# Performance work log

Hardware: AMD Instinct MI355X
Metric: run time of the kernel (lower is better)

Reference implementation:

```python
import jax, jax.numpy as jnp
import numpy as np

N = 100_000
E = 1_600_000
F_IN, D1, D2, D_EMB = 64, 32, 64, 64
NUM_GRAPHS = 16
BN_EPS = 1e-5


def _glorot(key, shape):
    fan_in, fan_out = shape[0], shape[1]
    lim = (6.0 / (fan_in + fan_out)) ** 0.5
    return jax.random.uniform(key, shape, jnp.float32, -lim, lim)


def setup_inputs() -> dict:
    key = jax.random.key(0)
    ks = jax.random.split(key, 12)
    x = jax.random.normal(ks[0], (N, F_IN), jnp.float32)
    edge_index = jax.random.randint(ks[1], (2, E), 0, N, jnp.int64)
    batch = jnp.sort(jax.random.randint(ks[2], (N,), 0, NUM_GRAPHS, jnp.int64))
    return {
        "x": x,
        "edge_index": edge_index,
        "batch": batch,
        "num_graphs": NUM_GRAPHS,
        "num_nodes": N,
        "W1a": _glorot(ks[3], (F_IN, D1)), "b1a": jnp.zeros((D1,), jnp.float32),
        "W1b": _glorot(ks[4], (D1, D2)), "b1b": jnp.zeros((D2,), jnp.float32),
        "g1": jnp.ones((D2,), jnp.float32), "be1": jnp.zeros((D2,), jnp.float32),
        "W2a": _glorot(ks[5], (D2, D2)), "b2a": jnp.zeros((D2,), jnp.float32),
        "W2b": _glorot(ks[6], (D2, D_EMB)), "b2b": jnp.zeros((D_EMB,), jnp.float32),
        "g2": jnp.ones((D_EMB,), jnp.float32), "be2": jnp.zeros((D_EMB,), jnp.float32),
    }


def _batchnorm_train(h, gamma, beta):
    mean = jnp.mean(h, axis=0)
    var = jnp.mean(jnp.square(h - mean), axis=0)  # biased var, as torch BN uses for normalization
    return (h - mean) * jax.lax.rsqrt(var + BN_EPS) * gamma + beta


def _gin_aggregate(x, src, dst, valid, n_nodes):
    # sum_{j in N(i)} x_j over valid edges only (masked scatter-add)
    msg = x[src] * valid[:, None]  # [E, D]
    return jax.ops.segment_sum(msg, dst, num_segments=n_nodes)


def reference(x, edge_index, batch, num_graphs, num_nodes,
              W1a, b1a, W1b, b1b, g1, be1,
              W2a, b2a, W2b, b2b, g2, be2):
    n_edges = edge_index.shape[1]
    per = n_edges // num_graphs
    # edge_mask: per-edge threshold g * num_nodes / num_graphs applied to both rows
    thresh = jnp.repeat(jnp.arange(num_graphs), per).astype(jnp.float32) * (num_nodes / num_graphs)
    valid = jnp.all(edge_index.astype(jnp.float32) - thresh[None, :] >= 0.0, axis=0)
    valid = valid.astype(x.dtype)
    src, dst = edge_index[0], edge_index[1]

    # GINConv 1 (eps=0): nn1(x + aggr)
    h = x + _gin_aggregate(x, src, dst, valid, num_nodes)
    h = jax.nn.relu(h @ W1a + b1a) @ W1b + b1b
    h = jax.nn.relu(h)
    h = _batchnorm_train(h, g1, be1)

    # GINConv 2
    h = h + _gin_aggregate(h, src, dst, valid, num_nodes)
    h = jax.nn.relu(h @ W2a + b2a) @ W2b + b2b
    h = jax.nn.relu(h)
    h = _batchnorm_train(h, g2, be2)

    # global_mean_pool
    sums = jax.ops.segment_sum(h, batch, num_segments=num_graphs)
    counts = jax.ops.segment_sum(jnp.ones((h.shape[0],), h.dtype), batch, num_segments=num_graphs)
    return sums / jnp.maximum(counts, 1.0)[:, None]
```

## Files before the change

### kernel.cpp

```cpp
#include <hip/hip_runtime.h>
#include <hip/hip_fp16.h>

#define NG 16
#define D 64
#define SLOT 32
#define NPB 128
#define INH 72

union HF4 { float4 f4; __half2 h2[4]; };
union HF2 { float2 f2; __half2 h2[2]; };

typedef _Float16 half4_t __attribute__((ext_vector_type(4)));
typedef float float4_t __attribute__((ext_vector_type(4)));

__device__ __forceinline__ float2 f2fma(float2 a, float2 b, float2 c) {
  return make_float2(fmaf(a.x, b.x, c.x), fmaf(a.y, b.y, c.y));
}
__device__ __forceinline__ float2 f2add(float2 a, float2 b) {
  return make_float2(a.x + b.x, a.y + b.y);
}

__global__ void prep_kernel(const float* __restrict__ x,
                            float2* __restrict__ xh, int n4,
                            float4* __restrict__ xz, float4* __restrict__ hz,
                            const int* __restrict__ ei,
                            int* __restrict__ fill, int* __restrict__ col,
                            int E, int per, int tmul) {
  int t = blockIdx.x * 256 + threadIdx.x;
  if (blockIdx.x == 0 && threadIdx.x < 16) {
    float4 z = make_float4(0.f, 0.f, 0.f, 0.f);
    if (threadIdx.x < 8) xz[threadIdx.x] = z;
    else hz[threadIdx.x - 8] = z;
  }
  if (t < n4) {
    float4 v = ((const float4*)x)[t];
    HF2 u;
    u.h2[0] = __floats2half2_rn(v.x, v.y);
    u.h2[1] = __floats2half2_rn(v.z, v.w);
    xh[t] = u.f2;
  }
  if (t < E) {
    int src = ei[t];
    int dst = ei[E + t];
    int thr = (t / per) * tmul;
    if (src >= thr && dst >= thr) {
      int k = atomicAdd(&fill[dst], 1);
      if (k < SLOT) col[dst * SLOT + k] = src;
    }
  }
}

template <int MID, bool FOLD_BN, int EPI>
__global__ __launch_bounds__(512, 2) void fused_layer_kernel(
    const float4* __restrict__ feat4,
    const int* __restrict__ col, const int* __restrict__ deg,
    const float* __restrict__ bn_sum, const float* __restrict__ bn_sq,
    const float* __restrict__ bn_gamma, const float* __restrict__ bn_beta,
    float invN,
    const float* __restrict__ Wa, const float* __restrict__ ba,
    const float* __restrict__ Wb, const float* __restrict__ bb,
    float2* __restrict__ out2,
    const int* __restrict__ batch,
    float* __restrict__ st_sum,
    float* __restrict__ st_sq,
    float* __restrict__ cnt,
    int N) {
  constexpr int CT = MID / 16;

  __shared__ __align__(16) __half s_h[NPB * INH];
  __shared__ __align__(16) __half s_wa[MID * 64];
  __shared__ __align__(16) __half s_wb[64 * MID];
  __shared__ __align__(16) float s_ba[MID];
  __shared__ __align__(16) float s_bb[D];
  __shared__ float s_bna[FOLD_BN ? D : 1];
  __shared__ float s_bnb[FOLD_BN ? D : 1];
  __shared__ int s_cnt[2];

  int tid = threadIdx.x;
  int base = blockIdx.x * NPB;

  {
    constexpr int WA_SLOTS = MID * 16;
    constexpr int WB_SLOTS = MID * 16;
    for (int g = tid; g < WA_SLOTS + WB_SLOTS; g += 512) {
      half4_t v;
      if (g < WA_SLOTS) {
        int l = g & 63, kt = (g >> 6) & 3, ct = g >> 8;
        int k0 = kt * 16 + ((l >> 4) << 2);
        int c = ct * 16 + (l & 15);
#pragma unroll
        for (int i = 0; i < 4; i++) v[i] = (_Float16)Wa[(k0 + i) * MID + c];
        *(half4_t*)&s_wa[g * 4] = v;
      } else {
        int g2 = g - WA_SLOTS;
        int l = g2 & 63;
        int kt = (g2 >> 6) & (CT - 1);
        int ot = g2 >> (6 + (CT == 4 ? 2 : 1));
        int k0 = kt * 16 + ((l >> 4) << 2);
        int o = ot * 16 + (l & 15);
#pragma unroll
        for (int i = 0; i < 4; i++) v[i] = (_Float16)Wb[(k0 + i) * D + o];
        *(half4_t*)&s_wb[g2 * 4] = v;
      }
    }
  }
  if (tid < MID) s_ba[tid] = ba[tid];
  if (tid < D) s_bb[tid] = bb[tid];
  if (FOLD_BN && tid < D) {
    float mean = bn_sum[tid] * invN;
    float var = bn_sq[tid] * invN - mean * mean;
    float av = bn_gamma[tid] * rsqrtf(var + 1e-5f);
    s_bna[tid] = av;
    s_bnb[tid] = bn_beta[tid] - mean * av;
  }
  if (EPI == 2 && tid < 2) s_cnt[tid] = 0;
  __syncthreads();

  {
    int q8 = tid & 7;
#pragma unroll
    for (int s0 = 0; s0 < 2; s0++) {
      int slot = (tid >> 3) + 64 * s0;
      int node = base + slot;
      float2 acc[4];
      if (node < N) {
        int d = min(deg[node], SLOT);
        const int* cl = col + node * SLOT;
        {
          HF4 s; s.f4 = feat4[(size_t)node * 8 + q8];
#pragma unroll
          for (int i = 0; i < 4; i++) acc[i] = __half22float2(s.h2[i]);
        }
        int dpad = (d + 15) & ~15;
        for (int j = 0; j < dpad; j += 16) {
          int4 sa = *(const int4*)(cl + j);
          int4 sb = *(const int4*)(cl + j + 4);
          int4 sc = *(const int4*)(cl + j + 8);
          int4 sd = *(const int4*)(cl + j + 12);
          int idx[16];
          idx[0]  = (j + 0  < d) ? sa.x : N;  idx[1]  = (j + 1  < d) ? sa.y : N;
          idx[2]  = (j + 2  < d) ? sa.z : N;  idx[3]  = (j + 3  < d) ? sa.w : N;
          idx[4]  = (j + 4  < d) ? sb.x : N;  idx[5]  = (j + 5  < d) ? sb.y : N;
          idx[6]  = (j + 6  < d) ? sb.z : N;  idx[7]  = (j + 7  < d) ? sb.w : N;
          idx[8]  = (j + 8  < d) ? sc.x : N;  idx[9]  = (j + 9  < d) ? sc.y : N;
          idx[10] = (j + 10 < d) ? sc.z : N;  idx[11] = (j + 11 < d) ? sc.w : N;
          idx[12] = (j + 12 < d) ? sd.x : N;  idx[13] = (j + 13 < d) ? sd.y : N;
          idx[14] = (j + 14 < d) ? sd.z : N;  idx[15] = (j + 15 < d) ? sd.w : N;
          HF4 u[16];
#pragma unroll
          for (int i = 0; i < 16; i++) u[i].f4 = feat4[(size_t)idx[i] * 8 + q8];
#pragma unroll
          for (int i = 0; i < 16; i++) {
#pragma unroll
            for (int c = 0; c < 4; c++)
              acc[c] = f2add(acc[c], __half22float2(u[i].h2[c]));
          }
        }
        if (FOLD_BN) {
          float dp = (float)(d + 1);
          int c0 = q8 * 8;
#pragma unroll
          for (int c = 0; c < 4; c++) {
            float2 a2 = *(const float2*)&s_bna[c0 + 2 * c];
            float2 b2 = *(const float2*)&s_bnb[c0 + 2 * c];
            acc[c] = f2fma(a2, acc[c], make_float2(dp * b2.x, dp * b2.y));
          }
        }
      } else {
#pragma unroll
        for (int i = 0; i < 4; i++) acc[i] = make_float2(0.f, 0.f);
      }
      HF4 o;
#pragma unroll
      for (int c = 0; c < 4; c++)
        o.h2[c] = __floats2half2_rn(acc[c].x, acc[c].y);
      *(float4*)&s_h[slot * INH + q8 * 8] = o.f4;
    }
  }
  __syncthreads();

  int w = tid >> 6;
  int l = tid & 63;
  int lg = l >> 4;
  int ln = l & 15;
  int nodeB = base + w * 16 + ln;

  half4_t hb[4];
#pragma unroll
  for (int kt = 0; kt < 4; kt++)
    hb[kt] = *(const half4_t*)&s_h[(w * 16 + ln) * INH + kt * 16 + lg * 4];

  float4_t c1[CT];
#pragma unroll
  for (int ct = 0; ct < CT; ct++) {
    c1[ct] = *(const float4_t*)&s_ba[ct * 16 + lg * 4];
#pragma unroll
    for (int kt = 0; kt < 4; kt++) {
      half4_t a = *(const half4_t*)&s_wa[((ct * 4 + kt) * 64 + l) * 4];
      c1[ct] = __builtin_amdgcn_mfma_f32_16x16x16f16(a, hb[kt], c1[ct], 0, 0, 0);
    }
  }
  half4_t mb[CT];
#pragma unroll
  for (int ct = 0; ct < CT; ct++) {
#pragma unroll
    for (int r = 0; r < 4; r++) mb[ct][r] = (_Float16)fmaxf(c1[ct][r], 0.f);
  }
  float4_t o4[4];
#pragma unroll
  for (int ot = 0; ot < 4; ot++) {
    o4[ot] = *(const float4_t*)&s_bb[ot * 16 + lg * 4];
#pragma unroll
    for (int kt = 0; kt < CT; kt++) {
      half4_t a = *(const half4_t*)&s_wb[((ot * CT + kt) * 64 + l) * 4];
      o4[ot] = __builtin_amdgcn_mfma_f32_16x16x16f16(a, mb[kt], o4[ot], 0, 0, 0);
    }
#pragma unroll
    for (int r = 0; r < 4; r++) o4[ot][r] = fmaxf(o4[ot][r], 0.f);
  }

  float* red = (float*)s_h;

  if (EPI == 1) {
    bool val = nodeB < N;
    if (val) {
#pragma unroll
      for (int ot = 0; ot < 4; ot++) {
        HF2 u;
        u.h2[0] = __floats2half2_rn(o4[ot][0], o4[ot][1]);
        u.h2[1] = __floats2half2_rn(o4[ot][2], o4[ot][3]);
        out2[(size_t)nodeB * 16 + ot * 4 + lg] = u.f2;
      }
    }
    float vm = val ? 1.f : 0.f;
#pragma unroll
    for (int ot = 0; ot < 4; ot++) {
      float4_t s, q;
#pragma unroll
      for (int r = 0; r < 4; r++) {
        float x = vm * o4[ot][r];
        s[r] = x; q[r] = x * o4[ot][r];
      }
#pragma unroll
      for (int m = 1; m < 16; m <<= 1) {
#pragma unroll
        for (int r = 0; r < 4; r++) {
          s[r] += __shfl_xor(s[r], m);
          q[r] += __shfl_xor(q[r], m);
        }
      }
      if (ln == 0) {
        *(float4_t*)&red[w * 576 + ot * 16 + lg * 4] = s;
        *(float4_t*)&red[w * 576 + 64 + ot * 16 + lg * 4] = q;
      }
    }
    __syncthreads();
    if (tid < D) {
      float s = 0.f, q = 0.f;
#pragma unroll
      for (int ww = 0; ww < 8; ww++) {
        s += red[ww * 576 + tid];
        q += red[ww * 576 + 64 + tid];
      }
      atomicAdd(&st_sum[tid], s);
      atomicAdd(&st_sq[tid], q);
    }
  }

  if (EPI == 2) {
    bool val = nodeB < N;
    int bl = val ? batch[nodeB] : -1;
    int g_lo = batch[base];
    int g_hi = batch[min(base + NPB - 1, N - 1)];
    float vm = val ? 1.f : 0.f;
    float wlo = (bl == g_lo) ? 1.f : 0.f;
    unsigned long long mlo = __ballot(lg == 0 && bl == g_lo);
    unsigned long long mhi = __ballot(lg == 0 && val && bl != g_lo);
    if (l == 0) {
      atomicAdd(&s_cnt[0], (int)__popcll(mlo));
      atomicAdd(&s_cnt[1], (int)__popcll(mhi));
    }
#pragma unroll
    for (int ot = 0; ot < 4; ot++) {
      float4_t sl, st, sq;
#pragma unroll
      for (int r = 0; r < 4; r++) {
        float x = vm * o4[ot][r];
        sl[r] = wlo * x;
        st[r] = x;
        sq[r] = x * o4[ot][r];
      }
#pragma unroll
      for (int m = 1; m < 16; m <<= 1) {
#pragma unroll
        for (int r = 0; r < 4; r++) {
          sl[r] += __shfl_xor(sl[r], m);
          st[r] += __shfl_xor(st[r], m);
          sq[r] += __shfl_xor(sq[r], m);
        }
      }
      if (ln == 0) {
        *(float4_t*)&red[w * 576 + ot * 16 + lg * 4] = sl;
        float4_t sh;
#pragma unroll
        for (int r = 0; r < 4; r++) sh[r] = st[r] - sl[r];
        *(float4_t*)&red[w * 576 + 64 + ot * 16 + lg * 4] = sh;
        *(float4_t*)&red[w * 576 + 128 + ot * 16 + lg * 4] = sq;
      }
    }
    __syncthreads();
    if (tid < D) {
      float sl = 0.f, sh = 0.f, sq = 0.f;
#pragma unroll
      for (int ww = 0; ww < 8; ww++) {
        sl += red[ww * 576 + tid];
        sh += red[ww * 576 + 64 + tid];
        sq += red[ww * 576 + 128 + tid];
      }
      atomicAdd(&st_sum[g_lo * D + tid], sl);
      if (g_hi != g_lo) atomicAdd(&st_sum[g_hi * D + tid], sh);
      atomicAdd(&st_sq[tid], sq);
    }
    if (tid == 0) {
      atomicAdd(&cnt[g_lo], (float)s_cnt[0]);
      if (g_hi != g_lo) atomicAdd(&cnt[g_hi], (float)s_cnt[1]);
    }
  }
}

__global__ void final_kernel(const float* __restrict__ pool,
                             const float* __restrict__ cnt,
                             const float* __restrict__ sq,
                             const float* __restrict__ gamma,
                             const float* __restrict__ beta,
                             float invN, float* __restrict__ out) {
  int c = threadIdx.x;
  float s = 0.f;
#pragma unroll
  for (int g = 0; g < NG; g++) s += pool[g * D + c];
  float mean = s * invN;
  float var = sq[c] * invN - mean * mean;
  float a = gamma[c] * rsqrtf(var + 1e-5f);
  float b = beta[c] - mean * a;
#pragma unroll
  for (int g = 0; g < NG; g++) {
    float n = cnt[g];
    out[g * D + c] = (a * pool[g * D + c] + n * b) / fmaxf(n, 1.f);
  }
}

extern "C" void kernel_launch(void* const* d_in, const int* in_sizes, int n_in,
                              void* d_out, int out_size, void* d_ws, size_t ws_size,
                              hipStream_t stream) {
  const float* x   = (const float*)d_in[0];
  const int* ei    = (const int*)d_in[1];
  const int* batch = (const int*)d_in[2];
  const float* W1a = (const float*)d_in[5];
  const float* b1a = (const float*)d_in[6];
  const float* W1b = (const float*)d_in[7];
  const float* b1b = (const float*)d_in[8];
  const float* g1  = (const float*)d_in[9];
  const float* be1 = (const float*)d_in[10];
  const float* W2a = (const float*)d_in[11];
  const float* b2a = (const float*)d_in[12];
  const float* W2b = (const float*)d_in[13];
  const float* b2b = (const float*)d_in[14];
  const float* g2  = (const float*)d_in[15];
  const float* be2 = (const float*)d_in[16];

  int N = in_sizes[0] / D;
  int E = in_sizes[1] / 2;
  int per = E / NG;
  int tmul = N / NG;
  float invN = 1.f / (float)N;

  float* ws = (float*)d_ws;
  size_t ndh = (size_t)(N + 1) * D / 2;
  float* h1h = ws;
  float* xh  = ws + ndh;
  int*   col = (int*)(ws + 2 * ndh);
  float* stats = ws + 2 * ndh + (size_t)N * SLOT;
  float* sum1 = stats;
  float* sq1  = stats + 64;
  float* pool = stats + 128;
  float* cnt  = stats + 128 + NG * D;
  float* sq2  = stats + 144 + NG * D;
  int*   fill = (int*)(stats + 208 + NG * D);

  hipMemsetAsync(stats, 0, (208 + NG * D + N) * sizeof(float), stream);

  int n4 = N * D / 4;
  int pgrid = (max(n4, E) + 255) / 256;
  prep_kernel<<<pgrid, 256, 0, stream>>>(
      x, (float2*)xh, n4,
      (float4*)(xh + (size_t)N * D / 2),
      (float4*)(h1h + (size_t)N * D / 2),
      ei, fill, col, E, per, tmul);

  int fblocks = (N + NPB - 1) / NPB;

  fused_layer_kernel<32, false, 1><<<fblocks, 512, 0, stream>>>(
      (const float4*)xh, col, fill, nullptr, nullptr, nullptr, nullptr, invN,
      W1a, b1a, W1b, b1b, (float2*)h1h, nullptr, sum1, sq1, nullptr, N);

  fused_layer_kernel<64, true, 2><<<fblocks, 512, 0, stream>>>(
      (const float4*)h1h, col, fill, sum1, sq1, g1, be1, invN,
      W2a, b2a, W2b, b2b, nullptr, batch, pool, sq2, cnt, N);

  final_kernel<<<1, 64, 0, stream>>>(pool, cnt, sq2, g2, be2, invN, (float*)d_out);
}
```

Measured before the change: 222.7 us.

## Prefetch neighbor gathers before weight staging and replace block reductions with banked atomics

Moves the column-list, degree and first 16 neighbor feature loads ahead of the weight staging into shared memory, so gather latency overlaps the setup work. The per-node degree masking is replaced by pre-filling the column table with a large sentinel that is clamped to the zero row, and a second batch of 16 is loaded only when some lane in the wave has degree above 16. The shared-memory reductions, and the barriers between the gather and MFMA stages, are removed; statistics are accumulated with per-wave atomics into 16 banks to spread contention. The cost is an extra memset of the full column table, more global atomics, and a manual lgkmcnt wait in place of a block barrier, which risks correctness if other waves' shared-memory rows are read before they are written.

Measured after the change: 326.6 us. 1.47x slower.

```diff
diff --git a/kernel.cpp b/kernel.cpp
--- a/kernel.cpp
+++ b/kernel.cpp
@@ -6,6 +6,7 @@
 #define SLOT 32
 #define NPB 128
 #define INH 72
+#define NBANK 16
 
 union HF4 { float4 f4; __half2 h2[4]; };
 union HF2 { float2 f2; __half2 h2[2]; };
@@ -18,6 +19,24 @@
 }
 __device__ __forceinline__ float2 f2add(float2 a, float2 b) {
   return make_float2(a.x + b.x, a.y + b.y);
+}
+
+__device__ __forceinline__ void load16(const float4* __restrict__ feat4, int N,
+                                       int q8, int4 a, int4 b, int4 c, int4 d,
+                                       HF4* u) {
+  int ix[16] = {a.x, a.y, a.z, a.w, b.x, b.y, b.z, b.w,
+                c.x, c.y, c.z, c.w, d.x, d.y, d.z, d.w};
+#pragma unroll
+  for (int i = 0; i < 16; i++)
+    u[i].f4 = feat4[(size_t)min(ix[i], N) * 8 + q8];
+}
+__device__ __forceinline__ void acc16(const HF4* u, float2* acc) {
+#pragma unroll
+  for (int i = 0; i < 16; i++) {
+#pragma unroll
+    for (int c = 0; c < 4; c++)
+      acc[c] = f2add(acc[c], __half22float2(u[i].h2[c]));
+  }
 }
 
 __global__ void prep_kernel(const float* __restrict__ x,
@@ -74,10 +93,34 @@
   __shared__ __align__(16) float s_bb[D];
   __shared__ float s_bna[FOLD_BN ? D : 1];
   __shared__ float s_bnb[FOLD_BN ? D : 1];
-  __shared__ int s_cnt[2];
 
   int tid = threadIdx.x;
+  int w = tid >> 6;
+  int l = tid & 63;
   int base = blockIdx.x * NPB;
+  int q8 = l & 7;
+  int s0 = w * 16 + (l >> 3);
+  int n0 = base + s0, n1 = n0 + 8;
+  int lg = l >> 4, ln = l & 15;
+  int nodeB = base + w * 16 + ln;
+
+  int a0 = min(n0, N - 1), a1 = min(n1, N - 1);
+  const int4* cp0 = (const int4*)(col + (size_t)a0 * SLOT);
+  const int4* cp1 = (const int4*)(col + (size_t)a1 * SLOT);
+  int4 cA0 = cp0[0], cB0 = cp0[1], cC0 = cp0[2], cD0 = cp0[3];
+  int4 cA1 = cp1[0], cB1 = cp1[1], cC1 = cp1[2], cD1 = cp1[3];
+  int d0 = deg[a0], d1 = deg[a1];
+  HF4 self0, self1;
+  self0.f4 = feat4[(size_t)min(n0, N) * 8 + q8];
+  self1.f4 = feat4[(size_t)min(n1, N) * 8 + q8];
+  int blB = 0, g_lo = 0, g_hi = 0;
+  if (EPI == 2) {
+    blB = batch[min(nodeB, N - 1)];
+    g_lo = batch[min(base + w * 16, N - 1)];
+    g_hi = batch[min(base + w * 16 + 15, N - 1)];
+  }
+  HF4 u0[16];
+  load16(feat4, N, q8, cA0, cB0, cC0, cD0, u0);
 
   {
     constexpr int WA_SLOTS = MID * 16;
@@ -85,19 +128,19 @@
     for (int g = tid; g < WA_SLOTS + WB_SLOTS; g += 512) {
       half4_t v;
       if (g < WA_SLOTS) {
-        int l = g & 63, kt = (g >> 6) & 3, ct = g >> 8;
-        int k0 = kt * 16 + ((l >> 4) << 2);
-        int c = ct * 16 + (l & 15);
+        int ll = g & 63, kt = (g >> 6) & 3, ct = g >> 8;
+        int k0 = kt * 16 + ((ll >> 4) << 2);
+        int c = ct * 16 + (ll & 15);
 #pragma unroll
         for (int i = 0; i < 4; i++) v[i] = (_Float16)Wa[(k0 + i) * MID + c];
         *(half4_t*)&s_wa[g * 4] = v;
       } else {
         int g2 = g - WA_SLOTS;
-        int l = g2 & 63;
+        int ll = g2 & 63;
         int kt = (g2 >> 6) & (CT - 1);
         int ot = g2 >> (6 + (CT == 4 ? 2 : 1));
-        int k0 = kt * 16 + ((l >> 4) << 2);
-        int o = ot * 16 + (l & 15);
+        int k0 = kt * 16 + ((ll >> 4) << 2);
+        int o = ot * 16 + (ll & 15);
 #pragma unroll
         for (int i = 0; i < 4; i++) v[i] = (_Float16)Wb[(k0 + i) * D + o];
         *(half4_t*)&s_wb[g2 * 4] = v;
@@ -107,83 +150,72 @@
   if (tid < MID) s_ba[tid] = ba[tid];
   if (tid < D) s_bb[tid] = bb[tid];
   if (FOLD_BN && tid < D) {
-    float mean = bn_sum[tid] * invN;
-    float var = bn_sq[tid] * invN - mean * mean;
+    float s = 0.f, q = 0.f;
+#pragma unroll
+    for (int b = 0; b < NBANK; b++) {
+      s += bn_sum[b * D + tid];
+      q += bn_sq[b * D + tid];
+    }
+    float mean = s * invN;
+    float var = q * invN - mean * mean;
     float av = bn_gamma[tid] * rsqrtf(var + 1e-5f);
     s_bna[tid] = av;
     s_bnb[tid] = bn_beta[tid] - mean * av;
   }
-  if (EPI == 2 && tid < 2) s_cnt[tid] = 0;
   __syncthreads();
 
   {
-    int q8 = tid & 7;
-#pragma unroll
-    for (int s0 = 0; s0 < 2; s0++) {
-      int slot = (tid >> 3) + 64 * s0;
-      int node = base + slot;
-      float2 acc[4];
-      if (node < N) {
-        int d = min(deg[node], SLOT);
-        const int* cl = col + node * SLOT;
-        {
-          HF4 s; s.f4 = feat4[(size_t)node * 8 + q8];
-#pragma unroll
-          for (int i = 0; i < 4; i++) acc[i] = __half22float2(s.h2[i]);
-        }
-        int dpad = (d + 15) & ~15;
-        for (int j = 0; j < dpad; j += 16) {
-          int4 sa = *(const int4*)(cl + j);
-          int4 sb = *(const int4*)(cl + j + 4);
-          int4 sc = *(const int4*)(cl + j + 8);
-          int4 sd = *(const int4*)(cl + j + 12);
-          int idx[16];
-          idx[0]  = (j + 0  < d) ? sa.x : N;  idx[1]  = (j + 1  < d) ? sa.y : N;
-          idx[2]  = (j + 2  < d) ? sa.z : N;  idx[3]  = (j + 3  < d) ? sa.w : N;
-          idx[4]  = (j + 4  < d) ? sb.x : N;  idx[5]  = (j + 5  < d) ? sb.y : N;
-          idx[6]  = (j + 6  < d) ? sb.z : N;  idx[7]  = (j + 7  < d) ? sb.w : N;
-          idx[8]  = (j + 8  < d) ? sc.x : N;  idx[9]  = (j + 9  < d) ? sc.y : N;
-          idx[10] = (j + 10 < d) ? sc.z : N;  idx[11] = (j + 11 < d) ? sc.w : N;
-          idx[12] = (j + 12 < d) ? sd.x : N;  idx[13] = (j + 13 < d) ? sd.y : N;
-          idx[14] = (j + 14 < d) ? sd.z : N;  idx[15] = (j + 15 < d) ? sd.w : N;
-          HF4 u[16];
-#pragma unroll
-          for (int i = 0; i < 16; i++) u[i].f4 = feat4[(size_t)idx[i] * 8 + q8];
-#pragma unroll
-          for (int i = 0; i < 16; i++) {
-#pragma unroll
-            for (int c = 0; c < 4; c++)
-              acc[c] = f2add(acc[c], __half22float2(u[i].h2[c]));
-          }
-        }
-        if (FOLD_BN) {
-          float dp = (float)(d + 1);
-          int c0 = q8 * 8;
-#pragma unroll
-          for (int c = 0; c < 4; c++) {
-            float2 a2 = *(const float2*)&s_bna[c0 + 2 * c];
-            float2 b2 = *(const float2*)&s_bnb[c0 + 2 * c];
-            acc[c] = f2fma(a2, acc[c], make_float2(dp * b2.x, dp * b2.y));
-          }
-        }
-      } else {
-#pragma unroll
-        for (int i = 0; i < 4; i++) acc[i] = make_float2(0.f, 0.f);
-      }
-      HF4 o;
-#pragma unroll
-      for (int c = 0; c < 4; c++)
-        o.h2[c] = __floats2half2_rn(acc[c].x, acc[c].y);
-      *(float4*)&s_h[slot * INH + q8 * 8] = o.f4;
-    }
-  }
-  __syncthreads();
-
-  int w = tid >> 6;
-  int l = tid & 63;
-  int lg = l >> 4;
-  int ln = l & 15;
-  int nodeB = base + w * 16 + ln;
+    float2 acc[4];
+#pragma unroll
+    for (int c = 0; c < 4; c++) acc[c] = __half22float2(self0.h2[c]);
+    acc16(u0, acc);
+    if (__any(d0 > 16)) {
+      HF4 t[16];
+      load16(feat4, N, q8, cp0[4], cp0[5], cp0[6], cp0[7], t);
+      acc16(t, acc);
+    }
+    if (FOLD_BN) {
+      float dp = (float)(min(d0, SLOT) + 1);
+      int c0 = q8 * 8;
+#pragma unroll
+      for (int c = 0; c < 4; c++) {
+        float2 a2 = *(const float2*)&s_bna[c0 + 2 * c];
+        float2 b2 = *(const float2*)&s_bnb[c0 + 2 * c];
+        acc[c] = f2fma(a2, acc[c], make_float2(dp * b2.x, dp * b2.y));
+      }
+    }
+    HF4 o;
+#pragma unroll
+    for (int c = 0; c < 4; c++) o.h2[c] = __floats2half2_rn(acc[c].x, acc[c].y);
+    *(float4*)&s_h[s0 * INH + q8 * 8] = o.f4;
+
+    HF4 u1[16];
+    load16(feat4, N, q8, cA1, cB1, cC1, cD1, u1);
+#pragma unroll
+    for (int c = 0; c < 4; c++) acc[c] = __half22float2(self1.h2[c]);
+    acc16(u1, acc);
+    if (__any(d1 > 16)) {
+      HF4 t[16];
+      load16(feat4, N, q8, cp1[4], cp1[5], cp1[6], cp1[7], t);
+      acc16(t, acc);
+    }
+    if (FOLD_BN) {
+      float dp = (float)(min(d1, SLOT) + 1);
+      int c0 = q8 * 8;
+#pragma unroll
+      for (int c = 0; c < 4; c++) {
+        float2 a2 = *(const float2*)&s_bna[c0 + 2 * c];
+        float2 b2 = *(const float2*)&s_bnb[c0 + 2 * c];
+        acc[c] = f2fma(a2, acc[c], make_float2(dp * b2.x, dp * b2.y));
+      }
+    }
+#pragma unroll
+    for (int c = 0; c < 4; c++) o.h2[c] = __floats2half2_rn(acc[c].x, acc[c].y);
+    *(float4*)&s_h[(s0 + 8) * INH + q8 * 8] = o.f4;
+  }
+
+  asm volatile("s_waitcnt lgkmcnt(0)" ::: "memory");
+  __builtin_amdgcn_sched_barrier(0);
 
   half4_t hb[4];
 #pragma unroll
@@ -219,7 +251,7 @@
     for (int r = 0; r < 4; r++) o4[ot][r] = fmaxf(o4[ot][r], 0.f);
   }
 
-  float* red = (float*)s_h;
+  int bank = ((blockIdx.x & 1) << 3) | w;
 
   if (EPI == 1) {
     bool val = nodeB < N;
@@ -238,8 +270,8 @@
       float4_t s, q;
 #pragma unroll
       for (int r = 0; r < 4; r++) {
-        float x = vm * o4[ot][r];
-        s[r] = x; q[r] = x * o4[ot][r];
+        float xx = vm * o4[ot][r];
+        s[r] = xx; q[r] = xx * o4[ot][r];
       }
 #pragma unroll
       for (int m = 1; m < 16; m <<= 1) {
@@ -250,45 +282,35 @@
         }
       }
       if (ln == 0) {
-        *(float4_t*)&red[w * 576 + ot * 16 + lg * 4] = s;
-        *(float4_t*)&red[w * 576 + 64 + ot * 16 + lg * 4] = q;
-      }
-    }
-    __syncthreads();
-    if (tid < D) {
-      float s = 0.f, q = 0.f;
-#pragma unroll
-      for (int ww = 0; ww < 8; ww++) {
-        s += red[ww * 576 + tid];
-        q += red[ww * 576 + 64 + tid];
-      }
-      atomicAdd(&st_sum[tid], s);
-      atomicAdd(&st_sq[tid], q);
+        int cb = ot * 16 + lg * 4;
+#pragma unroll
+        for (int r = 0; r < 4; r++) {
+          atomicAdd(&st_sum[bank * D + cb + r], s[r]);
+          atomicAdd(&st_sq[bank * D + cb + r], q[r]);
+        }
+      }
     }
   }
 
   if (EPI == 2) {
     bool val = nodeB < N;
-    int bl = val ? batch[nodeB] : -1;
-    int g_lo = batch[base];
-    int g_hi = batch[min(base + NPB - 1, N - 1)];
     float vm = val ? 1.f : 0.f;
-    float wlo = (bl == g_lo) ? 1.f : 0.f;
-    unsigned long long mlo = __ballot(lg == 0 && bl == g_lo);
-    unsigned long long mhi = __ballot(lg == 0 && val && bl != g_lo);
+    float wlo = (val && blB == g_lo) ? 1.f : 0.f;
+    unsigned long long mlo = __ballot(lg == 0 && val && blB == g_lo);
+    unsigned long long mhi = __ballot(lg == 0 && val && blB != g_lo);
     if (l == 0) {
-      atomicAdd(&s_cnt[0], (int)__popcll(mlo));
-      atomicAdd(&s_cnt[1], (int)__popcll(mhi));
+      atomicAdd(&cnt[g_lo], (float)__popcll(mlo));
+      if (g_hi != g_lo) atomicAdd(&cnt[g_hi], (float)__popcll(mhi));
     }
 #pragma unroll
     for (int ot = 0; ot < 4; ot++) {
       float4_t sl, st, sq;
 #pragma unroll
       for (int r = 0; r < 4; r++) {
-        float x = vm * o4[ot][r];
-        sl[r] = wlo * x;
-        st[r] = x;
-        sq[r] = x * o4[ot][r];
+        float xx = vm * o4[ot][r];
+        sl[r] = wlo * o4[ot][r];
+        st[r] = xx;
+        sq[r] = xx * o4[ot][r];
       }
 #pragma unroll
       for (int m = 1; m < 16; m <<= 1) {
@@ -300,30 +322,19 @@
         }
       }
       if (ln == 0) {
-        *(float4_t*)&red[w * 576 + ot * 16 + lg * 4] = sl;
-        float4_t sh;
-#pragma unroll
-        for (int r = 0; r < 4; r++) sh[r] = st[r] - sl[r];
-        *(float4_t*)&red[w * 576 + 64 + ot * 16 + lg * 4] = sh;
-        *(float4_t*)&red[w * 576 + 128 + ot * 16 + lg * 4] = sq;
-      }
-    }
-    __syncthreads();
-    if (tid < D) {
-      float sl = 0.f, sh = 0.f, sq = 0.f;
-#pragma unroll
-      for (int ww = 0; ww < 8; ww++) {
-        sl += red[ww * 576 + tid];
-        sh += red[ww * 576 + 64 + tid];
-        sq += red[ww * 576 + 128 + tid];
-      }
-      atomicAdd(&st_sum[g_lo * D + tid], sl);
-      if (g_hi != g_lo) atomicAdd(&st_sum[g_hi * D + tid], sh);
-      atomicAdd(&st_sq[tid], sq);
-    }
-    if (tid == 0) {
-      atomicAdd(&cnt[g_lo], (float)s_cnt[0]);
-      if (g_hi != g_lo) atomicAdd(&cnt[g_hi], (float)s_cnt[1]);
+        int cb = ot * 16 + lg * 4;
+#pragma unroll
+        for (int r = 0; r < 4; r++)
+          atomicAdd(&st_sum[g_lo * D + cb + r], sl[r]);
+        if (g_hi != g_lo) {
+#pragma unroll
+          for (int r = 0; r < 4; r++)
+            atomicAdd(&st_sum[g_hi * D + cb + r], st[r] - sl[r]);
+        }
+#pragma unroll
+        for (int r = 0; r < 4; r++)
+          atomicAdd(&st_sq[bank * D + cb + r], sq[r]);
+      }
     }
   }
 }
@@ -338,8 +349,11 @@
   float s = 0.f;
 #pragma unroll
   for (int g = 0; g < NG; g++) s += pool[g * D + c];
+  float q = 0.f;
+#pragma unroll
+  for (int b = 0; b < NBANK; b++) q += sq[b * D + c];
   float mean = s * invN;
-  float var = sq[c] * invN - mean * mean;
+  float var = q * invN - mean * mean;
   float a = gamma[c] * rsqrtf(var + 1e-5f);
   float b = beta[c] - mean * a;
 #pragma unroll
@@ -381,13 +395,15 @@
   int*   col = (int*)(ws + 2 * ndh);
   float* stats = ws + 2 * ndh + (size_t)N * SLOT;
   float* sum1 = stats;
-  float* sq1  = stats + 64;
-  float* pool = stats + 128;
-  float* cnt  = stats + 128 + NG * D;
-  float* sq2  = stats + 144 + NG * D;
-  int*   fill = (int*)(stats + 208 + NG * D);
-
-  hipMemsetAsync(stats, 0, (208 + NG * D + N) * sizeof(float), stream);
+  float* sq1  = stats + NBANK * D;
+  float* pool = stats + 2 * NBANK * D;
+  float* cnt  = pool + NG * D;
+  float* sq2  = cnt + NG;
+  int*   fill = (int*)(sq2 + NBANK * D);
+  size_t nstat = 3 * NBANK * D + NG * D + NG;
+
+  hipMemsetAsync(stats, 0, (nstat + N) * sizeof(float), stream);
+  hipMemsetAsync(col, 0x7F, (size_t)N * SLOT * sizeof(int), stream);
 
   int n4 = N * D / 4;
   int pgrid = (max(n4, E) + 255) / 256;
```
